# Kernel optimization log

Measured on AMD Instinct MI355X. Metric: run time of the kernel, lower is better.

## Reference

```python
import jax, jax.numpy as jnp
import numpy as np
from jax import lax

LAP = jnp.array([[1.0, 2.0, 1.0], [2.0, -12.0, 2.0], [1.0, 2.0, 1.0]], jnp.float32)
SOBEL_X = jnp.array([[-1.0, 0.0, 1.0], [-2.0, 0.0, 2.0], [-1.0, 0.0, 1.0]], jnp.float32)

GENE_SIZE = 3
UPDATE_RATE = 0.5
LEAKY_SLOPE = 0.01  # torch leaky_relu default


def _depthwise3x3_circular(x, k):
    # x: [B,C,H,W], k: [3,3]; circular pad then depthwise conv with same kernel per channel
    b, c, h, w = x.shape
    xp = jnp.pad(x, ((0, 0), (0, 0), (1, 1), (1, 1)), mode='wrap')
    kern = jnp.broadcast_to(k, (c, 1, 3, 3))
    return lax.conv_general_dilated(
        xp, kern, window_strides=(1, 1), padding='VALID',
        dimension_numbers=('NCHW', 'OIHW', 'NCHW'), feature_group_count=c)


def setup_inputs() -> dict:
    key = jax.random.key(0)
    k1, k2, k3, k4, k5 = jax.random.split(key, 5)
    chn, hidden_n, gene_size = 12, 128, 3
    perc_n = 3 * chn  # 36
    b, h, w = 16, 256, 256
    return {
        'x': jax.random.normal(k1, (b, chn, h, w), jnp.float32),
        'rand': jax.random.uniform(k2, (b, 1, h, w), jnp.float32),
        'w1_w': jax.random.normal(k3, (hidden_n, perc_n), jnp.float32) * 0.1,
        'w1_b': jax.random.normal(k4, (hidden_n,), jnp.float32) * 0.1,
        'w2_w': jax.random.normal(k5, (chn - gene_size, hidden_n), jnp.float32) * 0.1,
    }


def reference(x, rand, w1_w, w1_b, w2_w):
    b, c, h, w = x.shape
    gene = x[:, -GENE_SIZE:]
    # perception: ident (=x) and laplacian interleaved per channel, then gradient norm
    gx = _depthwise3x3_circular(x, SOBEL_X)
    gy = _depthwise3x3_circular(x, SOBEL_X.T)
    lap_x = _depthwise3x3_circular(x, LAP)
    state_lap = jnp.stack([x, lap_x], axis=2).reshape(b, 2 * c, h, w)  # [x0,lap0,x1,lap1,...]
    gradnorm = jnp.sqrt(gx * gx + gy * gy + 1e-8)
    perc = jnp.concatenate([state_lap, gradnorm], axis=1)  # [B, 3C, H, W]
    # 1x1 conv MLP
    y = jnp.einsum('bchw,oc->bohw', perc, w1_w) + w1_b[None, :, None, None]
    y = jax.nn.leaky_relu(y, LEAKY_SLOPE)
    y = jnp.einsum('bchw,oc->bohw', y, w2_w)  # [B, C-gene, H, W]
    # stochastic update mask
    update_mask = jnp.floor(rand + UPDATE_RATE)  # [B,1,H,W]
    # alive mask: 3x3 max pool (torch pads with -inf) on channel 3
    pool = lax.reduce_window(x[:, 3], -jnp.inf, lax.max,
                             (1, 3, 3), (1, 1, 1), [(0, 0), (1, 1), (1, 1)])
    life = (pool > 0.1)[:, None].astype(x.dtype)  # [B,1,H,W]
    x_new = x[:, :c - GENE_SIZE] + y * update_mask * life
    return jnp.concatenate([x_new, gene], axis=1)
```

## Files before the change

### kernel.cpp

```cpp
#include <hip/hip_runtime.h>
#include <hip/hip_bf16.h>
#include <math.h>

#define CHN  12
#define H    256
#define W    256
#define HID  128
#define OUTC 9
#define PSTR 56
#define YSTR 72

typedef __attribute__((ext_vector_type(4))) float    f32x4;
typedef __attribute__((ext_vector_type(8))) short    s16x8;
typedef __attribute__((ext_vector_type(4))) unsigned u32x4;
typedef __attribute__((ext_vector_type(8))) __bf16   bf16x8;

#define MFMA16x16x32(a, b, c) \
    __builtin_amdgcn_mfma_f32_16x16x32_bf16(__builtin_bit_cast(bf16x8, (a)), \
                                            __builtin_bit_cast(bf16x8, (b)), (c), 0, 0, 0)

static __device__ __forceinline__ unsigned short bfbits(float f) {
    __hip_bfloat16 h = __float2bfloat16(f);
    return __builtin_bit_cast(unsigned short, h);
}
static __device__ __forceinline__ float bits2f(unsigned short u) {
    __hip_bfloat16 h = __builtin_bit_cast(__hip_bfloat16, u);
    return __bfloat162float(h);
}
static __device__ __forceinline__ unsigned rna(float f) {
    return __builtin_bit_cast(unsigned, f) + 0x8000u;
}
static __device__ __forceinline__ unsigned pack2(unsigned uodd, unsigned ueven) {
    return __builtin_amdgcn_perm(uodd, ueven, 0x07060302u);
}
static __device__ __forceinline__ float fast_sqrtf(float x) {
    float r;
    asm("v_sqrt_f32 %0, %1" : "=v"(r) : "v"(x));
    return r;
}

__global__ void prep_weights(const float* __restrict__ w1w, const float* __restrict__ w1b,
                             const float* __restrict__ w2w, unsigned short* __restrict__ wsbuf)
{
    const int t = threadIdx.x;
    const int l = t & 63;
    const int grp = t >> 6;
    const int row = l & 15;
    const int g4 = l >> 4;
    unsigned short* wsa1  = wsbuf;
    unsigned short* wsa2p = wsbuf + 16 * 64 * 8;
    unsigned short* wsa2n = wsa2p + 4 * 64 * 8;

    for (int mf = grp; mf < 16; mf += 4) {
        int m = mf >> 1, f = mf & 1;
        int hid = m * 16 + row;
        for (int j = 0; j < 8; ++j) {
            int s = f * 32 + g4 * 8 + j;
            unsigned short v = 0;
            if (s < 36)       v = bfbits(w1w[hid * 36 + s]);
            else if (s < 48)  v = bfbits(w1w[hid * 36 + 2 * (s - 36) + 1]);
            else if (s == 48) v = bfbits(w1b[hid]);
            wsa1[(mf * 64 + l) * 8 + j] = v;
        }
    }
    {
        int kb = grp;
        for (int j = 0; j < 8; ++j) {
            float wv = (row < OUTC) ? w2w[row * HID + kb * 32 + g4 * 8 + j] : 0.f;
            wsa2p[(kb * 64 + l) * 8 + j] = bfbits(0.505f * wv);
            wsa2n[(kb * 64 + l) * 8 + j] = bfbits(0.495f * wv);
        }
    }
}

__global__ __launch_bounds__(256, 3) void nca_main(
    const float* __restrict__ x, const float* __restrict__ rnd,
    const unsigned short* __restrict__ wsbuf, float* __restrict__ out)
{
    __shared__ unsigned short perc_lds[W][PSTR];
    __shared__ unsigned short y1h[4][16][YSTR];

    const int t = threadIdx.x;
    const int orig = ((blockIdx.x & 7) << 9) | (blockIdx.x >> 3);
    const int h = orig & (H - 1);
    const int b = orig >> 8;
    const int hm = (h + H - 1) & (H - 1);
    const int hp = (h + 1) & (H - 1);
    const float* xb = x + (size_t)b * CHN * H * W;

    const int wm = (t + W - 1) & (W - 1);
    const int wp = (t + 1) & (W - 1);
    const float maskraw = rnd[((size_t)b * H + h) * W + t];

    float perc[36];
    float scale_reg = 0.f;
    #pragma unroll
    for (int c = 0; c < CHN; ++c) {
        const float* rm = xb + (size_t)c * H * W + (size_t)hm * W;
        const float* rc = xb + (size_t)c * H * W + (size_t)h  * W;
        const float* rp = xb + (size_t)c * H * W + (size_t)hp * W;
        float v00 = rm[wm], v01 = rm[t], v02 = rm[wp];
        float v10 = rc[wm], v11 = rc[t], v12 = rc[wp];
        float v20 = rp[wm], v21 = rp[t], v22 = rp[wp];

        float csm = fmaf(2.f, v10, v00) + v20;
        float csc = fmaf(2.f, v11, v01) + v21;
        float csp = fmaf(2.f, v12, v02) + v22;
        float gx  = csp - csm;
        float gy  = fmaf(2.f, v21 - v01, (v20 - v00) + (v22 - v02));
        float lap = fmaf(2.f, csc, csm + csp) - 16.f * v11;

        perc[2 * c]     = v11;
        perc[2 * c + 1] = lap;
        perc[24 + c]    = fast_sqrtf(fmaf(gx, gx, gy * gy) + 1e-8f);

        if (c == 3) {
            float cmm = v10, cmc = v11, cmp = v12;
            if (h > 0)     { cmm = fmaxf(cmm, v00); cmc = fmaxf(cmc, v01); cmp = fmaxf(cmp, v02); }
            if (h < H - 1) { cmm = fmaxf(cmm, v20); cmc = fmaxf(cmc, v21); cmp = fmaxf(cmp, v22); }
            float pool = cmc;
            if (t > 0)     pool = fmaxf(pool, cmm);
            if (t < W - 1) pool = fmaxf(pool, cmp);
            scale_reg = (pool > 0.1f && maskraw >= 0.5f) ? 1.f : 0.f;
        }
        if (c >= CHN - 3) {
            out[((size_t)b * CHN + c) * H * W + (size_t)h * W + t] = v11;
        }
    }

    {
        unsigned u[48];
        #pragma unroll
        for (int s = 0; s < 36; ++s) u[s] = rna(perc[s]);
        #pragma unroll
        for (int k = 0; k < 12; ++k) {
            float hif = __builtin_bit_cast(float, u[2 * k + 1] & 0xFFFF0000u);
            u[36 + k] = rna(perc[2 * k + 1] - hif);
        }
        unsigned short* prow = &perc_lds[t][0];
        #pragma unroll
        for (int g = 0; g < 6; ++g) {
            u32x4 v;
            #pragma unroll
            for (int j = 0; j < 4; ++j)
                v[j] = pack2(u[8 * g + 2 * j + 1], u[8 * g + 2 * j]);
            *(u32x4*)&prow[g * 8] = v;
        }
        u32x4 vpad;
        vpad[0] = 0x3F80u; vpad[1] = 0u; vpad[2] = 0u; vpad[3] = 0u;
        *(u32x4*)&prow[48] = vpad;
    }

    const int l = t & 63;
    const int wv = t >> 6;
    const int p16 = l & 15;
    const int g4 = l >> 4;
    const s16x8* A1  = (const s16x8*)wsbuf;
    const s16x8* A2P = A1 + 16 * 64;
    const s16x8* A2N = A2P + 4 * 64;

    s16x8 a1f[16];
    #pragma unroll
    for (int mf = 0; mf < 16; ++mf) a1f[mf] = A1[mf * 64 + l];
    s16x8 a2p[4], a2n[4];
    #pragma unroll
    for (int kb = 0; kb < 4; ++kb) { a2p[kb] = A2P[kb * 64 + l]; a2n[kb] = A2N[kb * 64 + l]; }

    const f32x4 fzero = {0.f, 0.f, 0.f, 0.f};

    #pragma unroll 1
    for (int pt = 0; pt < 4; ++pt) {
        const int p = wv * 64 + pt * 16 + p16;
        const unsigned short* prow = &perc_lds[p][0];
        s16x8 blo = *(const s16x8*)&prow[g4 * 8];
        s16x8 bhi;
        #pragma unroll
        for (int j = 0; j < 8; ++j) bhi[j] = 0;
        if (g4 < 3) bhi = *(const s16x8*)&prow[(4 + g4) * 8];

        unsigned short* ybase = &y1h[wv][p16][0];
        f32x4 acc2 = fzero;

        #pragma unroll
        for (int hh = 0; hh < 2; ++hh) {
            f32x4 acc[4];
            #pragma unroll
            for (int m2 = 0; m2 < 4; ++m2) {
                acc[m2] = MFMA16x16x32(a1f[(hh * 4 + m2) * 2],     blo, fzero);
                acc[m2] = MFMA16x16x32(a1f[(hh * 4 + m2) * 2 + 1], bhi, acc[m2]);
            }
            #pragma unroll
            for (int m2 = 0; m2 < 4; ++m2) {
                unsigned lo = pack2(rna(acc[m2][1]), rna(acc[m2][0]));
                unsigned hi = pack2(rna(acc[m2][3]), rna(acc[m2][2]));
                *(uint2*)(ybase + (2 * m2 + (g4 >> 1)) * 8 + (g4 & 1) * 4) = make_uint2(lo, hi);
            }
            #pragma unroll
            for (int kb2 = 0; kb2 < 2; ++kb2) {
                u32x4 bv = *(const u32x4*)(ybase + (kb2 * 4 + g4) * 8);
                u32x4 ba;
                #pragma unroll
                for (int j = 0; j < 4; ++j) ba[j] = bv[j] & 0x7FFF7FFFu;
                acc2 = MFMA16x16x32(a2p[hh * 2 + kb2], bv, acc2);
                acc2 = MFMA16x16x32(a2n[hh * 2 + kb2], ba, acc2);
            }
        }

        const float sc = __shfl(scale_reg, pt * 16 + p16, 64);
        const size_t pixbase = (size_t)b * CHN * H * W + (size_t)h * W + p;
        #pragma unroll
        for (int r = 0; r < 4; ++r) {
            int o = g4 * 4 + r;
            if (o < OUTC) {
                float xhi = bits2f((unsigned short)blo[2 * r]);
                out[pixbase + (size_t)o * H * W] = fmaf(acc2[r], sc, xhi);
            }
        }
    }
}

extern "C" void kernel_launch(void* const* d_in, const int* in_sizes, int n_in,
                              void* d_out, int out_size, void* d_ws, size_t ws_size,
                              hipStream_t stream) {
    const float* x   = (const float*)d_in[0];
    const float* rnd = (const float*)d_in[1];
    const float* w1w = (const float*)d_in[2];
    const float* w1b = (const float*)d_in[3];
    const float* w2w = (const float*)d_in[4];
    float* out = (float*)d_out;
    unsigned short* ws = (unsigned short*)d_ws;

    prep_weights<<<dim3(1), dim3(256), 0, stream>>>(w1w, w1b, w2w, ws);
    nca_main<<<dim3(16 * 256), dim3(256), 0, stream>>>(x, rnd, ws, out);
}
```

Baseline: 58.11 us.

## Split rows into 64-wide single-wave blocks and apply leaky ReLU explicitly

Each block now handles a quarter image row with one 64-thread wavefront instead of a full row with four waves. This shrinks shared memory per block and quadruples the grid, aiming at finer scheduling and higher occupancy. The leaky ReLU is now applied in VALU before packing to bf16, so the second layer needs one MFMA per k-block instead of the 0.505/0.495 abs-split pair. That halves the layer-2 MFMAs and the weight registers, at the cost of a few extra VALU max ops and more per-block overhead from reloading weights in four times as many blocks.

```diff
diff --git a/kernel.cpp b/kernel.cpp
--- a/kernel.cpp
+++ b/kernel.cpp
@@ -47,9 +47,8 @@
     const int grp = t >> 6;
     const int row = l & 15;
     const int g4 = l >> 4;
-    unsigned short* wsa1  = wsbuf;
-    unsigned short* wsa2p = wsbuf + 16 * 64 * 8;
-    unsigned short* wsa2n = wsa2p + 4 * 64 * 8;
+    unsigned short* wsa1 = wsbuf;
+    unsigned short* wsa2 = wsbuf + 16 * 64 * 8;
 
     for (int mf = grp; mf < 16; mf += 4) {
         int m = mf >> 1, f = mf & 1;
@@ -67,30 +66,32 @@
         int kb = grp;
         for (int j = 0; j < 8; ++j) {
             float wv = (row < OUTC) ? w2w[row * HID + kb * 32 + g4 * 8 + j] : 0.f;
-            wsa2p[(kb * 64 + l) * 8 + j] = bfbits(0.505f * wv);
-            wsa2n[(kb * 64 + l) * 8 + j] = bfbits(0.495f * wv);
-        }
-    }
-}
-
-__global__ __launch_bounds__(256, 3) void nca_main(
+            wsa2[(kb * 64 + l) * 8 + j] = bfbits(wv);
+        }
+    }
+}
+
+__global__ __launch_bounds__(64, 4) void nca_main(
     const float* __restrict__ x, const float* __restrict__ rnd,
     const unsigned short* __restrict__ wsbuf, float* __restrict__ out)
 {
-    __shared__ unsigned short perc_lds[W][PSTR];
-    __shared__ unsigned short y1h[4][16][YSTR];
+    __shared__ unsigned short perc_lds[64][PSTR];
+    __shared__ unsigned short y1h[16][YSTR];
 
     const int t = threadIdx.x;
-    const int orig = ((blockIdx.x & 7) << 9) | (blockIdx.x >> 3);
-    const int h = orig & (H - 1);
-    const int b = orig >> 8;
+    const int orig = ((blockIdx.x & 7) << 11) | (blockIdx.x >> 3);
+    const int q   = orig & 3;
+    const int row = orig >> 2;
+    const int h = row & (H - 1);
+    const int b = row >> 8;
+    const int col = q * 64 + t;
     const int hm = (h + H - 1) & (H - 1);
     const int hp = (h + 1) & (H - 1);
     const float* xb = x + (size_t)b * CHN * H * W;
 
-    const int wm = (t + W - 1) & (W - 1);
-    const int wp = (t + 1) & (W - 1);
-    const float maskraw = rnd[((size_t)b * H + h) * W + t];
+    const int wm = (col + W - 1) & (W - 1);
+    const int wp = (col + 1) & (W - 1);
+    const float maskraw = rnd[((size_t)b * H + h) * W + col];
 
     float perc[36];
     float scale_reg = 0.f;
@@ -99,9 +100,9 @@
         const float* rm = xb + (size_t)c * H * W + (size_t)hm * W;
         const float* rc = xb + (size_t)c * H * W + (size_t)h  * W;
         const float* rp = xb + (size_t)c * H * W + (size_t)hp * W;
-        float v00 = rm[wm], v01 = rm[t], v02 = rm[wp];
-        float v10 = rc[wm], v11 = rc[t], v12 = rc[wp];
-        float v20 = rp[wm], v21 = rp[t], v22 = rp[wp];
+        float v00 = rm[wm], v01 = rm[col], v02 = rm[wp];
+        float v10 = rc[wm], v11 = rc[col], v12 = rc[wp];
+        float v20 = rp[wm], v21 = rp[col], v22 = rp[wp];
 
         float csm = fmaf(2.f, v10, v00) + v20;
         float csc = fmaf(2.f, v11, v01) + v21;
@@ -119,12 +120,12 @@
             if (h > 0)     { cmm = fmaxf(cmm, v00); cmc = fmaxf(cmc, v01); cmp = fmaxf(cmp, v02); }
             if (h < H - 1) { cmm = fmaxf(cmm, v20); cmc = fmaxf(cmc, v21); cmp = fmaxf(cmp, v22); }
             float pool = cmc;
-            if (t > 0)     pool = fmaxf(pool, cmm);
-            if (t < W - 1) pool = fmaxf(pool, cmp);
+            if (col > 0)     pool = fmaxf(pool, cmm);
+            if (col < W - 1) pool = fmaxf(pool, cmp);
             scale_reg = (pool > 0.1f && maskraw >= 0.5f) ? 1.f : 0.f;
         }
         if (c >= CHN - 3) {
-            out[((size_t)b * CHN + c) * H * W + (size_t)h * W + t] = v11;
+            out[((size_t)b * CHN + c) * H * W + (size_t)h * W + col] = v11;
         }
     }
 
@@ -151,26 +152,23 @@
         *(u32x4*)&prow[48] = vpad;
     }
 
-    const int l = t & 63;
-    const int wv = t >> 6;
-    const int p16 = l & 15;
-    const int g4 = l >> 4;
-    const s16x8* A1  = (const s16x8*)wsbuf;
-    const s16x8* A2P = A1 + 16 * 64;
-    const s16x8* A2N = A2P + 4 * 64;
+    const int p16 = t & 15;
+    const int g4 = t >> 4;
+    const s16x8* A1 = (const s16x8*)wsbuf;
+    const s16x8* A2 = A1 + 16 * 64;
 
     s16x8 a1f[16];
     #pragma unroll
-    for (int mf = 0; mf < 16; ++mf) a1f[mf] = A1[mf * 64 + l];
-    s16x8 a2p[4], a2n[4];
+    for (int mf = 0; mf < 16; ++mf) a1f[mf] = A1[mf * 64 + t];
+    s16x8 a2[4];
     #pragma unroll
-    for (int kb = 0; kb < 4; ++kb) { a2p[kb] = A2P[kb * 64 + l]; a2n[kb] = A2N[kb * 64 + l]; }
+    for (int kb = 0; kb < 4; ++kb) a2[kb] = A2[kb * 64 + t];
 
     const f32x4 fzero = {0.f, 0.f, 0.f, 0.f};
 
     #pragma unroll 1
     for (int pt = 0; pt < 4; ++pt) {
-        const int p = wv * 64 + pt * 16 + p16;
+        const int p = pt * 16 + p16;
         const unsigned short* prow = &perc_lds[p][0];
         s16x8 blo = *(const s16x8*)&prow[g4 * 8];
         s16x8 bhi;
@@ -178,7 +176,7 @@
         for (int j = 0; j < 8; ++j) bhi[j] = 0;
         if (g4 < 3) bhi = *(const s16x8*)&prow[(4 + g4) * 8];
 
-        unsigned short* ybase = &y1h[wv][p16][0];
+        unsigned short* ybase = &y1h[p16][0];
         f32x4 acc2 = fzero;
 
         #pragma unroll
@@ -191,23 +189,23 @@
             }
             #pragma unroll
             for (int m2 = 0; m2 < 4; ++m2) {
-                unsigned lo = pack2(rna(acc[m2][1]), rna(acc[m2][0]));
-                unsigned hi = pack2(rna(acc[m2][3]), rna(acc[m2][2]));
+                float w0 = fmaxf(acc[m2][0], 0.01f * acc[m2][0]);
+                float w1 = fmaxf(acc[m2][1], 0.01f * acc[m2][1]);
+                float w2 = fmaxf(acc[m2][2], 0.01f * acc[m2][2]);
+                float w3 = fmaxf(acc[m2][3], 0.01f * acc[m2][3]);
+                unsigned lo = pack2(rna(w1), rna(w0));
+                unsigned hi = pack2(rna(w3), rna(w2));
                 *(uint2*)(ybase + (2 * m2 + (g4 >> 1)) * 8 + (g4 & 1) * 4) = make_uint2(lo, hi);
             }
             #pragma unroll
             for (int kb2 = 0; kb2 < 2; ++kb2) {
-                u32x4 bv = *(const u32x4*)(ybase + (kb2 * 4 + g4) * 8);
-                u32x4 ba;
-                #pragma unroll
-                for (int j = 0; j < 4; ++j) ba[j] = bv[j] & 0x7FFF7FFFu;
-                acc2 = MFMA16x16x32(a2p[hh * 2 + kb2], bv, acc2);
-                acc2 = MFMA16x16x32(a2n[hh * 2 + kb2], ba, acc2);
-            }
-        }
-
-        const float sc = __shfl(scale_reg, pt * 16 + p16, 64);
-        const size_t pixbase = (size_t)b * CHN * H * W + (size_t)h * W + p;
+                u32x4 b2 = *(const u32x4*)(ybase + (kb2 * 4 + g4) * 8);
+                acc2 = MFMA16x16x32(a2[hh * 2 + kb2], b2, acc2);
+            }
+        }
+
+        const float sc = __shfl(scale_reg, p, 64);
+        const size_t pixbase = (size_t)b * CHN * H * W + (size_t)h * W + (q * 64 + p);
         #pragma unroll
         for (int r = 0; r < 4; ++r) {
             int o = g4 * 4 + r;
@@ -231,5 +229,5 @@
     unsigned short* ws = (unsigned short*)d_ws;
 
     prep_weights<<<dim3(1), dim3(256), 0, stream>>>(w1w, w1b, w2w, ws);
-    nca_main<<<dim3(16 * 256), dim3(256), 0, stream>>>(x, rnd, ws, out);
-}
+    nca_main<<<dim3(16 * 256 * 4), dim3(64), 0, stream>>>(x, rnd, ws, out);
+}
```

Result: slower. 59.69 us (+2.7%).
